# Kernel optimization log

Hardware: AMD Instinct MI355X
Metric: run time of the kernel (lower is better)

## Reference

```python
import jax, jax.numpy as jnp
import numpy as np

B, T, K, D, V = 32, 200, 50, 100, 500000


def setup_inputs() -> dict:
    key = jax.random.key(0)
    k_ids, k_emb, k_wht, k_bht, k_wrel, k_brel = jax.random.split(key, 6)
    ids = jax.random.randint(k_ids, (B, T, K, 3), 0, V, dtype=jnp.int64)
    emb = jax.random.normal(k_emb, (V, D), dtype=jnp.float32) * 0.02
    # torch Linear weights are [out_features, in_features]
    W_ht = jax.random.normal(k_wht, (D, 2 * D), dtype=jnp.float32) * 0.05
    b_ht = jax.random.normal(k_bht, (D,), dtype=jnp.float32) * 0.05
    W_rel = jax.random.normal(k_wrel, (D, D), dtype=jnp.float32) * 0.05
    b_rel = jax.random.normal(k_brel, (D,), dtype=jnp.float32) * 0.05
    return {
        "batch_size": B,
        "one_two_triples_id": ids,
        "one_two_triple_num": T,
        "emb": emb,
        "W_ht": W_ht,
        "b_ht": b_ht,
        "W_rel": W_rel,
        "b_rel": b_rel,
    }


def reference(batch_size, one_two_triples_id, one_two_triple_num, emb, W_ht, b_ht, W_rel, b_rel):
    d = emb.shape[1]
    # gather: [B, T, K, 3, d] -> [B, T, K, 3d]
    tri = emb[one_two_triples_id].reshape(batch_size, one_two_triple_num, -1, 3 * d)
    head, relation, tail = jnp.split(tri, 3, axis=3)          # each [B,T,K,d]
    head_tail = jnp.concatenate([head, tail], axis=3)          # [B,T,K,2d]
    ht_t = jnp.tanh(jnp.einsum('btkf,df->btkd', head_tail, W_ht) + b_ht)
    rel_t = jnp.einsum('btke,de->btkd', relation, W_rel) + b_rel
    e_weight = jnp.sum(rel_t * ht_t, axis=3)                   # [B,T,K]
    alpha = jax.nn.softmax(e_weight, axis=2)                   # softmax over triples K
    one_two_embed = jnp.sum(alpha[..., None] * head_tail, axis=2)  # [B,T,2d]
    return one_two_embed
```

## Files before the change

### kernel.cpp

```cpp
#include <hip/hip_runtime.h>
#include <hip/hip_bf16.h>

#define KK 50
#define DD 100
#define TWO_D 200
#define DPAD 112
#define KHT 224
#define KRL 128

#define NROWS 150
#define TP 104
#define SX_BYTES 32768
#define NCH_RAW (NROWS * 25)

#define WS_FLAGS 0
#define WS_WHT 256
#define WS_WRL (WS_WHT + DPAD*KHT*2)
#define WS_BHT (WS_WRL + DPAD*KRL*2)
#define WS_BRL (WS_BHT + 256)

typedef __attribute__((ext_vector_type(8))) short        s8v;
typedef __attribute__((ext_vector_type(8))) __bf16       b8v;
typedef __attribute__((ext_vector_type(4))) __bf16       b4v;
typedef __attribute__((ext_vector_type(4))) float        f32x4;

template <typename T>
__device__ __forceinline__ auto mfma_try(T a, T b, f32x4 c, int)
    -> decltype(__builtin_amdgcn_mfma_f32_16x16x32_bf16(a, b, c, 0, 0, 0)) {
    return __builtin_amdgcn_mfma_f32_16x16x32_bf16(a, b, c, 0, 0, 0);
}
template <typename T, typename U = b8v>
__device__ __forceinline__ f32x4 mfma_try(T a, T b, f32x4 c, long) {
    U ab = __builtin_bit_cast(U, a);
    U bb = __builtin_bit_cast(U, b);
    return __builtin_amdgcn_mfma_f32_16x16x32_bf16(ab, bb, c, 0, 0, 0);
}
__device__ __forceinline__ f32x4 mfma16x16x32_bf16(s8v a, s8v b, f32x4 c) {
    return mfma_try(a, b, c, 0);
}

__device__ __forceinline__ float bf2f(__hip_bfloat16 h) { return __bfloat162float(h); }

__device__ __forceinline__ float tanh_fast(float x) {
    float e = __expf(2.f * x);
    return 1.f - 2.f * __builtin_amdgcn_rcpf(e + 1.f);
}

__global__ void detect_dtypes(const unsigned int* __restrict__ emb_raw,
                              const unsigned int* __restrict__ ids_raw,
                              int* __restrict__ flags) {
    const int lane = threadIdx.x;
    int f32 = 0;
    #pragma unroll
    for (int rep = 0; rep < 4; rep++) {
        unsigned int w = emb_raw[lane + rep * 64];
        unsigned int e0 = (w >> 7)  & 0xFF;
        unsigned int e1 = (w >> 23) & 0xFF;
        if (e0 >= 0x87 || e1 >= 0x87) f32 = 1;
    }
    unsigned long long mf = __ballot(f32 != 0);
    unsigned long long mz = __ballot(ids_raw[2 * lane + 1] == 0u);
    if (lane == 0) {
        flags[0] = mf ? 1 : 0;
        flags[1] = (__popcll(mz) >= 32) ? 1 : 0;
    }
}

__global__ void prep_weights(const void* __restrict__ Wht, const void* __restrict__ bht,
                             const void* __restrict__ Wrl, const void* __restrict__ brl,
                             void* __restrict__ ws) {
    const int* flags = (const int*)ws;
    const bool f32 = flags[0] != 0;
    __hip_bfloat16* whtp = (__hip_bfloat16*)((char*)ws + WS_WHT);
    __hip_bfloat16* wrlp = (__hip_bfloat16*)((char*)ws + WS_WRL);
    __hip_bfloat16* bhtp = (__hip_bfloat16*)((char*)ws + WS_BHT);
    __hip_bfloat16* brlp = (__hip_bfloat16*)((char*)ws + WS_BRL);

    const int gid = blockIdx.x * blockDim.x + threadIdx.x;
    const int gs  = gridDim.x * blockDim.x;

    for (int i = gid; i < DPAD * KHT; i += gs) {
        int d = i / KHT, f = i - d * KHT;
        int src = -1;
        if (f < 112) { if (f < DD) src = f; }
        else { int t = f - 112; if (t < DD) src = DD + t; }
        float v = 0.f;
        if (d < DD && src >= 0)
            v = f32 ? ((const float*)Wht)[d * TWO_D + src]
                    : bf2f(((const __hip_bfloat16*)Wht)[d * TWO_D + src]);
        whtp[i] = __float2bfloat16(v);
    }
    for (int i = gid; i < DPAD * KRL; i += gs) {
        int d = i / KRL, f = i - d * KRL;
        float v = 0.f;
        if (d < DD && f < DD)
            v = f32 ? ((const float*)Wrl)[d * DD + f]
                    : bf2f(((const __hip_bfloat16*)Wrl)[d * DD + f]);
        wrlp[i] = __float2bfloat16(v);
    }
    for (int i = gid; i < DPAD; i += gs) {
        float vh = 0.f, vr = 0.f;
        if (i < DD) {
            vh = f32 ? ((const float*)bht)[i] : bf2f(((const __hip_bfloat16*)bht)[i]);
            vr = f32 ? ((const float*)brl)[i] : bf2f(((const __hip_bfloat16*)brl)[i]);
        }
        bhtp[i] = __float2bfloat16(vh);
        brlp[i] = __float2bfloat16(vr);
    }
}

template <int CNT>
__device__ __forceinline__ void gather_f32(const float* __restrict__ embf,
                                           const int* __restrict__ sIds,
                                           char* __restrict__ sX, int tid, int base) {
    float4 v[CNT];
    int doff[CNT];
    #pragma unroll
    for (int i = 0; i < CNT; ++i) {
        int c = tid + (base + i) * 256;
        bool ok = (c < NCH_RAW);
        int cc = ok ? c : 0;
        int seg = cc / 25;
        int off = (cc - seg * 25) * 4;
        size_t id = (size_t)sIds[seg];
        v[i] = *(const float4*)(embf + id * DD + off);
        doff[i] = ok ? (seg * (TP * 2) + off * 2) : -1;
    }
    #pragma unroll
    for (int i = 0; i < CNT; ++i) {
        if (doff[i] >= 0) {
            b4v pk = { (__bf16)v[i].x, (__bf16)v[i].y, (__bf16)v[i].z, (__bf16)v[i].w };
            *(b4v*)(sX + doff[i]) = pk;
        }
    }
}

template <int CNT>
__device__ __forceinline__ void gather_b16raw(const __hip_bfloat16* __restrict__ embh,
                                              const int* __restrict__ sIds,
                                              char* __restrict__ sX, int tid, int base) {
    uint2 v[CNT];
    int doff[CNT];
    #pragma unroll
    for (int i = 0; i < CNT; ++i) {
        int c = tid + (base + i) * 256;
        bool ok = (c < NCH_RAW);
        int cc = ok ? c : 0;
        int seg = cc / 25;
        int off = (cc - seg * 25) * 4;
        size_t id = (size_t)sIds[seg];
        v[i] = *(const uint2*)(embh + id * DD + off);
        doff[i] = ok ? (seg * (TP * 2) + off * 2) : -1;
    }
    #pragma unroll
    for (int i = 0; i < CNT; ++i) {
        if (doff[i] >= 0) *(uint2*)(sX + doff[i]) = v[i];
    }
}

__global__ __launch_bounds__(256, 4) void fused_outer_encoder(
    const int* __restrict__ ids,
    const void* __restrict__ emb_raw,
    const void* __restrict__ ws,
    float* __restrict__ out)
{
    __shared__ char  sX[SX_BYTES];
    __shared__ int   sIds[NROWS];
    __shared__ float sEp[4][64];
    __shared__ float sAl[64];

    const int* flags = (const int*)ws;
    const __hip_bfloat16* whtp = (const __hip_bfloat16*)((const char*)ws + WS_WHT);
    const __hip_bfloat16* wrlp = (const __hip_bfloat16*)((const char*)ws + WS_WRL);
    const __hip_bfloat16* bhtp = (const __hip_bfloat16*)((const char*)ws + WS_BHT);
    const __hip_bfloat16* brlp = (const __hip_bfloat16*)((const char*)ws + WS_BRL);

    const int tid = threadIdx.x;
    const int bt  = blockIdx.x;
    const bool f32      = flags[0] != 0;
    const int idsStride = flags[1] ? 2 : 1;

    int myid = 0;
    if (tid < NROWS) myid = ids[(bt * NROWS + tid) * idsStride];

    for (int i = tid; i < 346; i += 256) {
        int byteoff = (i < 150) ? (i * (TP * 2) + 200) : (NROWS * (TP * 2) + (i - 150) * 8);
        *(uint2*)(sX + byteoff) = make_uint2(0u, 0u);
    }
    if (tid < NROWS) sIds[tid] = myid;
    __syncthreads();

    if (f32) {
        const float* embf = (const float*)emb_raw;
        gather_f32<8>(embf, sIds, sX, tid, 0);
        gather_f32<7>(embf, sIds, sX, tid, 8);
    } else {
        const __hip_bfloat16* embh = (const __hip_bfloat16*)emb_raw;
        gather_b16raw<8>(embh, sIds, sX, tid, 0);
        gather_b16raw<7>(embh, sIds, sX, tid, 8);
    }
    __syncthreads();

    const int lane = tid & 63;
    const int w    = tid >> 6;
    const int n    = lane & 15;
    const int q    = lane >> 4;
    const int nt0  = (w < 3) ? 2 * w : 6;
    const int nt1  = (w < 3) ? 2 * w + 1 : 6;
    const float m1 = (w < 3) ? 1.f : 0.f;

    const __hip_bfloat16* sxe = (const __hip_bfloat16*)sX;

    int hb[4];
    #pragma unroll
    for (int m = 0; m < 4; m++) {
        int ar = m * 16 + n;
        ar = (ar < KK) ? ar : (KK - 1);
        hb[m] = 3 * ar * TP;
    }

    f32x4 accH[4][2];
    #pragma unroll
    for (int m = 0; m < 4; m++)
        #pragma unroll
        for (int t = 0; t < 2; t++)
            #pragma unroll
            for (int j = 0; j < 4; j++) accH[m][t][j] = 0.f;

    #pragma unroll
    for (int ks = 0; ks < 7; ks++) {
        const int c    = ks * 4 + q;
        const int aoff = (c < 14) ? (c * 8) : (2 * TP + (c - 14) * 8);
        s8v b0 = *(const s8v*)(whtp + (nt0 * 16 + n) * KHT + ks * 32 + q * 8);
        s8v b1 = *(const s8v*)(whtp + (nt1 * 16 + n) * KHT + ks * 32 + q * 8);
        #pragma unroll
        for (int m = 0; m < 4; m++) {
            s8v a = *(const s8v*)(sxe + hb[m] + aoff);
            accH[m][0] = mfma16x16x32_bf16(a, b0, accH[m][0]);
            accH[m][1] = mfma16x16x32_bf16(a, b1, accH[m][1]);
        }
    }

    const float bh0 = bf2f(bhtp[nt0 * 16 + n]);
    const float bh1 = bf2f(bhtp[nt1 * 16 + n]);
    float htv[4][2][4];
    #pragma unroll
    for (int m = 0; m < 4; m++)
        #pragma unroll
        for (int j = 0; j < 4; j++) {
            htv[m][0][j] = tanh_fast(accH[m][0][j] + bh0);
            htv[m][1][j] = tanh_fast(accH[m][1][j] + bh1);
        }

    f32x4 accR[4][2];
    #pragma unroll
    for (int m = 0; m < 4; m++)
        #pragma unroll
        for (int t = 0; t < 2; t++)
            #pragma unroll
            for (int j = 0; j < 4; j++) accR[m][t][j] = 0.f;

    #pragma unroll
    for (int ks = 0; ks < 4; ks++) {
        const int c    = ks * 4 + q;
        const int aoff = TP + c * 8;
        s8v b0 = *(const s8v*)(wrlp + (nt0 * 16 + n) * KRL + ks * 32 + q * 8);
        s8v b1 = *(const s8v*)(wrlp + (nt1 * 16 + n) * KRL + ks * 32 + q * 8);
        #pragma unroll
        for (int m = 0; m < 4; m++) {
            s8v a = *(const s8v*)(sxe + hb[m] + aoff);
            accR[m][0] = mfma16x16x32_bf16(a, b0, accR[m][0]);
            accR[m][1] = mfma16x16x32_bf16(a, b1, accR[m][1]);
        }
    }

    const float br0 = bf2f(brlp[nt0 * 16 + n]);
    const float br1 = bf2f(brlp[nt1 * 16 + n]);
    float dj[4][4];
    #pragma unroll
    for (int m = 0; m < 4; m++)
        #pragma unroll
        for (int j = 0; j < 4; j++)
            dj[m][j] = (accR[m][0][j] + br0) * htv[m][0][j]
                     + m1 * (accR[m][1][j] + br1) * htv[m][1][j];

    #pragma unroll
    for (int mask = 1; mask < 16; mask <<= 1)
        #pragma unroll
        for (int m = 0; m < 4; m++)
            #pragma unroll
            for (int j = 0; j < 4; j++)
                dj[m][j] += __shfl_xor(dj[m][j], mask, 64);

    if (n == 0) {
        #pragma unroll
        for (int m = 0; m < 4; m++)
            #pragma unroll
            for (int j = 0; j < 4; j++)
                sEp[w][m * 16 + q * 4 + j] = dj[m][j];
    }
    __syncthreads();

    if (tid < 64) {
        float e = sEp[0][tid] + sEp[1][tid] + sEp[2][tid] + sEp[3][tid];
        float v = (tid < KK) ? e : -3.0e38f;
        float mx = v;
        #pragma unroll
        for (int mask = 1; mask < 64; mask <<= 1) mx = fmaxf(mx, __shfl_xor(mx, mask, 64));
        float p = (tid < KK) ? __expf(v - mx) : 0.f;
        float s = p;
        #pragma unroll
        for (int mask = 1; mask < 64; mask <<= 1) s += __shfl_xor(s, mask, 64);
        if (tid < KK) sAl[tid] = p / s;
    }
    __syncthreads();

    if (tid < TWO_D) {
        const int half  = tid / DD;
        const int dmod  = tid - half * DD;
        const int roff  = half ? 2 : 0;
        float acc = 0.f;
        #pragma unroll 10
        for (int k = 0; k < KK; k++)
            acc += sAl[k] * bf2f(sxe[(3 * k + roff) * TP + dmod]);
        out[(size_t)bt * TWO_D + tid] = acc;
    }
}

extern "C" void kernel_launch(void* const* d_in, const int* in_sizes, int n_in,
                              void* d_out, int out_size, void* d_ws, size_t ws_size,
                              hipStream_t stream) {
    const int*  ids = (const int*)d_in[1];
    const void* emb = d_in[3];
    const void* Wht = d_in[4];
    const void* bht = d_in[5];
    const void* Wrl = d_in[6];
    const void* brl = d_in[7];
    float* out = (float*)d_out;

    const int nbt = in_sizes[1] / NROWS;

    hipLaunchKernelGGL(detect_dtypes, dim3(1), dim3(64), 0, stream,
                       (const unsigned int*)emb, (const unsigned int*)ids, (int*)d_ws);
    hipLaunchKernelGGL(prep_weights, dim3(64), dim3(256), 0, stream,
                       Wht, bht, Wrl, brl, d_ws);
    hipLaunchKernelGGL(fused_outer_encoder, dim3(nbt), dim3(256), 0, stream,
                       ids, emb, (const void*)d_ws, out);
}
```

Before: 362.6 us.

## Fold dtype detection into weight prep and raise occupancy via LDS aliasing

Merges the dtype-detect kernel into prep_weights, so every block recomputes the flags locally and one kernel launch goes away. In the main kernel, sIds, sEp and sAl now alias a trimmed shared buffer, so LDS per block drops to about 32.5KB. The M-tile loop is split into two sequential passes of two tiles each, which lowers register pressure, and launch bounds are raised to 5 blocks per CU. The trade-off is less instruction-level parallelism per wave, and sIds/sEp share memory, which relies on the barriers between gather and use.

```diff
diff --git a/kernel.cpp b/kernel.cpp
--- a/kernel.cpp
+++ b/kernel.cpp
@@ -10,7 +10,10 @@
 
 #define NROWS 150
 #define TP 104
-#define SX_BYTES 32768
+#define SX_DATA 31232
+#define SEP_OFF 31232
+#define SAL_OFF 32256
+#define SX_TOTAL 32512
 #define NCH_RAW (NROWS * 25)
 
 #define WS_FLAGS 0
@@ -46,37 +49,42 @@
     return 1.f - 2.f * __builtin_amdgcn_rcpf(e + 1.f);
 }
 
-__global__ void detect_dtypes(const unsigned int* __restrict__ emb_raw,
-                              const unsigned int* __restrict__ ids_raw,
-                              int* __restrict__ flags) {
-    const int lane = threadIdx.x;
-    int f32 = 0;
-    #pragma unroll
-    for (int rep = 0; rep < 4; rep++) {
-        unsigned int w = emb_raw[lane + rep * 64];
-        unsigned int e0 = (w >> 7)  & 0xFF;
-        unsigned int e1 = (w >> 23) & 0xFF;
-        if (e0 >= 0x87 || e1 >= 0x87) f32 = 1;
-    }
-    unsigned long long mf = __ballot(f32 != 0);
-    unsigned long long mz = __ballot(ids_raw[2 * lane + 1] == 0u);
-    if (lane == 0) {
-        flags[0] = mf ? 1 : 0;
-        flags[1] = (__popcll(mz) >= 32) ? 1 : 0;
-    }
-}
-
 __global__ void prep_weights(const void* __restrict__ Wht, const void* __restrict__ bht,
                              const void* __restrict__ Wrl, const void* __restrict__ brl,
+                             const unsigned int* __restrict__ emb_raw,
+                             const unsigned int* __restrict__ ids_raw,
                              void* __restrict__ ws) {
-    const int* flags = (const int*)ws;
-    const bool f32 = flags[0] != 0;
+    __shared__ int sFlags[2];
+    const int tid = threadIdx.x;
+    if (tid < 64) {
+        int f32d = 0;
+        #pragma unroll
+        for (int rep = 0; rep < 4; rep++) {
+            unsigned int wd = emb_raw[tid + rep * 64];
+            unsigned int e0 = (wd >> 7)  & 0xFF;
+            unsigned int e1 = (wd >> 23) & 0xFF;
+            if (e0 >= 0x87 || e1 >= 0x87) f32d = 1;
+        }
+        unsigned long long mf = __ballot(f32d != 0);
+        unsigned long long mz = __ballot(ids_raw[2 * tid + 1] == 0u);
+        if (tid == 0) {
+            sFlags[0] = mf ? 1 : 0;
+            sFlags[1] = (__popcll(mz) >= 32) ? 1 : 0;
+        }
+    }
+    __syncthreads();
+    const bool f32 = sFlags[0] != 0;
+    if (blockIdx.x == 0 && tid == 0) {
+        ((int*)ws)[0] = sFlags[0];
+        ((int*)ws)[1] = sFlags[1];
+    }
+
     __hip_bfloat16* whtp = (__hip_bfloat16*)((char*)ws + WS_WHT);
     __hip_bfloat16* wrlp = (__hip_bfloat16*)((char*)ws + WS_WRL);
     __hip_bfloat16* bhtp = (__hip_bfloat16*)((char*)ws + WS_BHT);
     __hip_bfloat16* brlp = (__hip_bfloat16*)((char*)ws + WS_BRL);
 
-    const int gid = blockIdx.x * blockDim.x + threadIdx.x;
+    const int gid = blockIdx.x * blockDim.x + tid;
     const int gs  = gridDim.x * blockDim.x;
 
     for (int i = gid; i < DPAD * KHT; i += gs) {
@@ -158,16 +166,16 @@
     }
 }
 
-__global__ __launch_bounds__(256, 4) void fused_outer_encoder(
+__global__ __launch_bounds__(256, 5) void fused_outer_encoder(
     const int* __restrict__ ids,
     const void* __restrict__ emb_raw,
     const void* __restrict__ ws,
     float* __restrict__ out)
 {
-    __shared__ char  sX[SX_BYTES];
-    __shared__ int   sIds[NROWS];
-    __shared__ float sEp[4][64];
-    __shared__ float sAl[64];
+    __shared__ char sX[SX_TOTAL];
+    int*   sIds = (int*)(sX + SEP_OFF);
+    float* sEp  = (float*)(sX + SEP_OFF);
+    float* sAl  = (float*)(sX + SAL_OFF);
 
     const int* flags = (const int*)ws;
     const __hip_bfloat16* whtp = (const __hip_bfloat16*)((const char*)ws + WS_WHT);
@@ -183,8 +191,8 @@
     int myid = 0;
     if (tid < NROWS) myid = ids[(bt * NROWS + tid) * idsStride];
 
-    for (int i = tid; i < 346; i += 256) {
-        int byteoff = (i < 150) ? (i * (TP * 2) + 200) : (NROWS * (TP * 2) + (i - 150) * 8);
+    for (int i = tid; i < 154; i += 256) {
+        int byteoff = (i < 150) ? (i * (TP * 2) + 200) : (31200 + (i - 150) * 8);
         *(uint2*)(sX + byteoff) = make_uint2(0u, 0u);
     }
     if (tid < NROWS) sIds[tid] = myid;
@@ -210,99 +218,100 @@
     const float m1 = (w < 3) ? 1.f : 0.f;
 
     const __hip_bfloat16* sxe = (const __hip_bfloat16*)sX;
-
-    int hb[4];
-    #pragma unroll
-    for (int m = 0; m < 4; m++) {
-        int ar = m * 16 + n;
-        ar = (ar < KK) ? ar : (KK - 1);
-        hb[m] = 3 * ar * TP;
-    }
-
-    f32x4 accH[4][2];
-    #pragma unroll
-    for (int m = 0; m < 4; m++)
-        #pragma unroll
-        for (int t = 0; t < 2; t++)
-            #pragma unroll
-            for (int j = 0; j < 4; j++) accH[m][t][j] = 0.f;
-
-    #pragma unroll
-    for (int ks = 0; ks < 7; ks++) {
-        const int c    = ks * 4 + q;
-        const int aoff = (c < 14) ? (c * 8) : (2 * TP + (c - 14) * 8);
-        s8v b0 = *(const s8v*)(whtp + (nt0 * 16 + n) * KHT + ks * 32 + q * 8);
-        s8v b1 = *(const s8v*)(whtp + (nt1 * 16 + n) * KHT + ks * 32 + q * 8);
-        #pragma unroll
-        for (int m = 0; m < 4; m++) {
-            s8v a = *(const s8v*)(sxe + hb[m] + aoff);
-            accH[m][0] = mfma16x16x32_bf16(a, b0, accH[m][0]);
-            accH[m][1] = mfma16x16x32_bf16(a, b1, accH[m][1]);
-        }
-    }
-
     const float bh0 = bf2f(bhtp[nt0 * 16 + n]);
     const float bh1 = bf2f(bhtp[nt1 * 16 + n]);
-    float htv[4][2][4];
-    #pragma unroll
-    for (int m = 0; m < 4; m++)
-        #pragma unroll
-        for (int j = 0; j < 4; j++) {
-            htv[m][0][j] = tanh_fast(accH[m][0][j] + bh0);
-            htv[m][1][j] = tanh_fast(accH[m][1][j] + bh1);
-        }
-
-    f32x4 accR[4][2];
-    #pragma unroll
-    for (int m = 0; m < 4; m++)
-        #pragma unroll
-        for (int t = 0; t < 2; t++)
-            #pragma unroll
-            for (int j = 0; j < 4; j++) accR[m][t][j] = 0.f;
-
-    #pragma unroll
-    for (int ks = 0; ks < 4; ks++) {
-        const int c    = ks * 4 + q;
-        const int aoff = TP + c * 8;
-        s8v b0 = *(const s8v*)(wrlp + (nt0 * 16 + n) * KRL + ks * 32 + q * 8);
-        s8v b1 = *(const s8v*)(wrlp + (nt1 * 16 + n) * KRL + ks * 32 + q * 8);
-        #pragma unroll
-        for (int m = 0; m < 4; m++) {
-            s8v a = *(const s8v*)(sxe + hb[m] + aoff);
-            accR[m][0] = mfma16x16x32_bf16(a, b0, accR[m][0]);
-            accR[m][1] = mfma16x16x32_bf16(a, b1, accR[m][1]);
-        }
-    }
-
     const float br0 = bf2f(brlp[nt0 * 16 + n]);
     const float br1 = bf2f(brlp[nt1 * 16 + n]);
-    float dj[4][4];
-    #pragma unroll
-    for (int m = 0; m < 4; m++)
-        #pragma unroll
-        for (int j = 0; j < 4; j++)
-            dj[m][j] = (accR[m][0][j] + br0) * htv[m][0][j]
-                     + m1 * (accR[m][1][j] + br1) * htv[m][1][j];
-
-    #pragma unroll
-    for (int mask = 1; mask < 16; mask <<= 1)
-        #pragma unroll
-        for (int m = 0; m < 4; m++)
+
+    #pragma unroll 1
+    for (int mp = 0; mp < 2; mp++) {
+        int ar0 = mp * 32 + n;      if (ar0 >= KK) ar0 = KK - 1;
+        int ar1 = mp * 32 + 16 + n; if (ar1 >= KK) ar1 = KK - 1;
+        const int hb0 = 3 * ar0 * TP;
+        const int hb1 = 3 * ar1 * TP;
+
+        f32x4 accH[2][2];
+        #pragma unroll
+        for (int mi = 0; mi < 2; mi++)
+            #pragma unroll
+            for (int t = 0; t < 2; t++)
+                #pragma unroll
+                for (int j = 0; j < 4; j++) accH[mi][t][j] = 0.f;
+
+        #pragma unroll
+        for (int ks = 0; ks < 7; ks++) {
+            const int c    = ks * 4 + q;
+            const int aoff = (c < 14) ? (c * 8) : (2 * TP + (c - 14) * 8);
+            s8v b0 = *(const s8v*)(whtp + (nt0 * 16 + n) * KHT + ks * 32 + q * 8);
+            s8v b1 = *(const s8v*)(whtp + (nt1 * 16 + n) * KHT + ks * 32 + q * 8);
+            s8v a0 = *(const s8v*)(sxe + hb0 + aoff);
+            s8v a1 = *(const s8v*)(sxe + hb1 + aoff);
+            accH[0][0] = mfma16x16x32_bf16(a0, b0, accH[0][0]);
+            accH[0][1] = mfma16x16x32_bf16(a0, b1, accH[0][1]);
+            accH[1][0] = mfma16x16x32_bf16(a1, b0, accH[1][0]);
+            accH[1][1] = mfma16x16x32_bf16(a1, b1, accH[1][1]);
+        }
+
+        float htv[2][2][4];
+        #pragma unroll
+        for (int mi = 0; mi < 2; mi++)
+            #pragma unroll
+            for (int j = 0; j < 4; j++) {
+                htv[mi][0][j] = tanh_fast(accH[mi][0][j] + bh0);
+                htv[mi][1][j] = tanh_fast(accH[mi][1][j] + bh1);
+            }
+
+        f32x4 accR[2][2];
+        #pragma unroll
+        for (int mi = 0; mi < 2; mi++)
+            #pragma unroll
+            for (int t = 0; t < 2; t++)
+                #pragma unroll
+                for (int j = 0; j < 4; j++) accR[mi][t][j] = 0.f;
+
+        #pragma unroll
+        for (int ks = 0; ks < 4; ks++) {
+            const int c    = ks * 4 + q;
+            const int aoff = TP + c * 8;
+            s8v b0 = *(const s8v*)(wrlp + (nt0 * 16 + n) * KRL + ks * 32 + q * 8);
+            s8v b1 = *(const s8v*)(wrlp + (nt1 * 16 + n) * KRL + ks * 32 + q * 8);
+            s8v a0 = *(const s8v*)(sxe + hb0 + aoff);
+            s8v a1 = *(const s8v*)(sxe + hb1 + aoff);
+            accR[0][0] = mfma16x16x32_bf16(a0, b0, accR[0][0]);
+            accR[0][1] = mfma16x16x32_bf16(a0, b1, accR[0][1]);
+            accR[1][0] = mfma16x16x32_bf16(a1, b0, accR[1][0]);
+            accR[1][1] = mfma16x16x32_bf16(a1, b1, accR[1][1]);
+        }
+
+        float dj[2][4];
+        #pragma unroll
+        for (int mi = 0; mi < 2; mi++)
             #pragma unroll
             for (int j = 0; j < 4; j++)
-                dj[m][j] += __shfl_xor(dj[m][j], mask, 64);
-
-    if (n == 0) {
-        #pragma unroll
-        for (int m = 0; m < 4; m++)
-            #pragma unroll
-            for (int j = 0; j < 4; j++)
-                sEp[w][m * 16 + q * 4 + j] = dj[m][j];
+                dj[mi][j] = (accR[mi][0][j] + br0) * htv[mi][0][j]
+                          + m1 * (accR[mi][1][j] + br1) * htv[mi][1][j];
+
+        #pragma unroll
+        for (int mask = 1; mask < 16; mask <<= 1)
+            #pragma unroll
+            for (int mi = 0; mi < 2; mi++)
+                #pragma unroll
+                for (int j = 0; j < 4; j++)
+                    dj[mi][j] += __shfl_xor(dj[mi][j], mask, 64);
+
+        if (n == 0) {
+            #pragma unroll
+            for (int mi = 0; mi < 2; mi++)
+                #pragma unroll
+                for (int j = 0; j < 4; j++)
+                    sEp[w * 64 + mp * 32 + mi * 16 + q * 4 + j] = dj[mi][j];
+        }
     }
     __syncthreads();
 
     if (tid < 64) {
-        float e = sEp[0][tid] + sEp[1][tid] + sEp[2][tid] + sEp[3][tid];
+        float e = sEp[0 * 64 + tid] + sEp[1 * 64 + tid]
+                + sEp[2 * 64 + tid] + sEp[3 * 64 + tid];
         float v = (tid < KK) ? e : -3.0e38f;
         float mx = v;
         #pragma unroll
@@ -340,10 +349,9 @@
 
     const int nbt = in_sizes[1] / NROWS;
 
-    hipLaunchKernelGGL(detect_dtypes, dim3(1), dim3(64), 0, stream,
-                       (const unsigned int*)emb, (const unsigned int*)ids, (int*)d_ws);
     hipLaunchKernelGGL(prep_weights, dim3(64), dim3(256), 0, stream,
-                       Wht, bht, Wrl, brl, d_ws);
+                       Wht, bht, Wrl, brl,
+                       (const unsigned int*)emb, (const unsigned int*)ids, d_ws);
     hipLaunchKernelGGL(fused_outer_encoder, dim3(nbt), dim3(256), 0, stream,
                        ids, emb, (const void*)d_ws, out);
 }
```

Measured after the change: 497.2 us. 37.1% more time.
